# Performance work log

Measured on AMD Instinct MI355X. Metric: run time of the kernel, lower is better.

The kernel has to match this reference:

```python
import jax, jax.numpy as jnp
import numpy as np

N_EMBED = 1024
N_HEAD = 16
HEAD_DIM = N_EMBED // N_HEAD


def setup_inputs() -> dict:
    key = jax.random.key(0)
    ks = jax.random.split(key, 6)
    B, T, C = 4, 2048, N_EMBED
    scale = 1.0 / np.sqrt(C)
    x = jax.random.normal(ks[0], (B, T, C), dtype=jnp.float32)
    # torch nn.Linear weights are [out, in]; y = x @ W.T
    Wk = jax.random.normal(ks[1], (C, C), dtype=jnp.float32) * scale
    Wq = jax.random.normal(ks[2], (C, C), dtype=jnp.float32) * scale
    Wv = jax.random.normal(ks[3], (C, C), dtype=jnp.float32) * scale
    Wp = jax.random.normal(ks[4], (C, C), dtype=jnp.float32) * scale
    bp = jax.random.normal(ks[5], (C,), dtype=jnp.float32) * 0.01
    return {"x": x, "Wk": Wk, "Wq": Wq, "Wv": Wv, "Wp": Wp, "bp": bp}


def reference(x, Wk, Wq, Wv, Wp, bp):
    B, T, C = x.shape
    H, D = N_HEAD, HEAD_DIM
    # QKV projections (torch Linear: x @ W.T), split heads -> [B, H, T, D]
    k = (x @ Wk.T).reshape(B, T, H, D).transpose(0, 2, 1, 3)
    q = (x @ Wq.T).reshape(B, T, H, D).transpose(0, 2, 1, 3)
    v = (x @ Wv.T).reshape(B, T, H, D).transpose(0, 2, 1, 3)
    # scaled scores [B, H, T, T]
    att = jnp.einsum('bhtd,bhsd->bhts', q, k) * (1.0 / np.sqrt(D))
    causal = jnp.tril(jnp.ones((T, T), dtype=bool))
    att = jnp.where(causal[None, None, :, :], att, -jnp.inf)
    att = jax.nn.softmax(att, axis=-1)
    out = jnp.einsum('bhts,bhsd->bhtd', att, v)  # [B, H, T, D]
    out = out.transpose(0, 2, 1, 3).reshape(B, T, C)
    out = out @ Wp.T + bp
    return out
```

## Files before the change

### kernel.cpp

```cpp
#include <hip/hip_runtime.h>

typedef __bf16 bf16_t;
typedef bf16_t bf16x4 __attribute__((ext_vector_type(4)));
typedef bf16_t bf16x8 __attribute__((ext_vector_type(8)));
typedef float f32x4 __attribute__((ext_vector_type(4)));

#define B_ 4
#define T_ 2048
#define C_ 1024
#define H_ 16
#define D_ 64

#define GLDS(g, l)                                                          \
  __builtin_amdgcn_global_load_lds(                                         \
      (const __attribute__((address_space(1))) void*)(g),                   \
      (__attribute__((address_space(3))) void*)(l), 16, 0, 0)

static __device__ __forceinline__ f32x4 mfma16(bf16x8 a, bf16x8 b, f32x4 c) {
  return __builtin_amdgcn_mfma_f32_16x16x32_bf16(a, b, c, 0, 0, 0);
}

static __device__ __forceinline__ float exp2_hw(float x) {
  float r;
  asm("v_exp_f32 %0, %1" : "=v"(r) : "v"(x));
  return r;
}

__global__ void cvt_all(const float* __restrict__ x, const float* __restrict__ wq,
                        const float* __restrict__ wk, const float* __restrict__ wv,
                        const float* __restrict__ wp, bf16_t* __restrict__ xb,
                        bf16_t* __restrict__ wqb, bf16_t* __restrict__ wkb,
                        bf16_t* __restrict__ wvb, bf16_t* __restrict__ wpb) {
  int i = blockIdx.x * blockDim.x + threadIdx.x;
  const float* src;
  bf16_t* dst;
  int off;
  if (i < 2097152) {
    src = x; dst = xb; off = i;
  } else {
    int r = i - 2097152;
    int region = r >> 18;
    off = r & 262143;
    if (region == 0) { src = wq; dst = wqb; }
    else if (region == 1) { src = wk; dst = wkb; }
    else if (region == 2) { src = wv; dst = wvb; }
    else { src = wp; dst = wpb; }
  }
  float4 v = ((const float4*)src)[off];
  bf16x4 o = {(bf16_t)v.x, (bf16_t)v.y, (bf16_t)v.z, (bf16_t)v.w};
  ((bf16x4*)dst)[off] = o;
}

__global__ __launch_bounds__(512) void gemm_qkv(
    const bf16_t* __restrict__ xb, const bf16_t* __restrict__ wq,
    const bf16_t* __restrict__ wk, const bf16_t* __restrict__ wv,
    bf16_t* __restrict__ qo, bf16_t* __restrict__ ko, bf16_t* __restrict__ vt) {
  __shared__ bf16_t lA[2][128 * 64];
  __shared__ bf16_t lB[2][3][128 * 64];
  const int tid = threadIdx.x, wave = tid >> 6, lane = tid & 63;
  const int g = lane >> 4;
  const int bid = blockIdx.x;
  const int swz = ((bid & 7) << 6) | (bid >> 3);
  const int col0 = (swz & 7) * 128, row0 = (swz >> 3) * 128;
  const int wr = wave >> 2, wc = wave & 3;
  f32x4 acc[3][4][2] = {};

  const int soff[2] = {wave * 1024, (8 + wave) * 1024};
  size_t sgo[2];
#pragma unroll
  for (int i = 0; i < 2; ++i) {
    const int lin = soff[i] + lane * 16;
    const int r = lin >> 7;
    const int c = ((lin >> 4) & 7) ^ (r & 7);
    sgo[i] = (size_t)r * C_ + c * 8;
  }

#define QKV_STAGE(k0, b)                                                    \
  {                                                                         \
    _Pragma("unroll") for (int i = 0; i < 2; ++i) {                         \
      GLDS(xb + (size_t)row0 * C_ + (k0) + sgo[i], &lA[b][soff[i] >> 1]);   \
      GLDS(wq + (size_t)col0 * C_ + (k0) + sgo[i], &lB[b][0][soff[i] >> 1]);\
      GLDS(wk + (size_t)col0 * C_ + (k0) + sgo[i], &lB[b][1][soff[i] >> 1]);\
      GLDS(wv + (size_t)col0 * C_ + (k0) + sgo[i], &lB[b][2][soff[i] >> 1]);\
    }                                                                       \
  }

  QKV_STAGE(0, 0);
  int cur = 0;
  for (int k0 = 0; k0 < C_; k0 += 64) {
    __syncthreads();
    if (k0 + 64 < C_) QKV_STAGE(k0 + 64, cur ^ 1);
#pragma unroll
    for (int s = 0; s < 2; ++s) {
      const int c = s * 4 + g;
      bf16x8 af[4];
#pragma unroll
      for (int m = 0; m < 4; ++m) {
        const int r = wr * 64 + m * 16 + (lane & 15);
        af[m] = *(const bf16x8*)((const char*)lA[cur] + r * 128 +
                                 ((c ^ (r & 7)) << 4));
      }
#pragma unroll
      for (int z = 0; z < 3; ++z) {
        bf16x8 bfr[2];
#pragma unroll
        for (int n = 0; n < 2; ++n) {
          const int r = wc * 32 + n * 16 + (lane & 15);
          bfr[n] = *(const bf16x8*)((const char*)lB[cur][z] + r * 128 +
                                    ((c ^ (r & 7)) << 4));
        }
#pragma unroll
        for (int m = 0; m < 4; ++m)
#pragma unroll
          for (int n = 0; n < 2; ++n)
            acc[z][m][n] = mfma16(af[m], bfr[n], acc[z][m][n]);
      }
    }
    cur ^= 1;
  }
#pragma unroll
  for (int z = 0; z < 3; ++z) {
    bf16_t* outb = (z == 0) ? qo : ((z == 1) ? ko : vt);
    const float qs = (z == 0) ? 0.125f * 1.4426950408889634f : 1.0f;
#pragma unroll
    for (int m = 0; m < 4; ++m) {
#pragma unroll
      for (int n = 0; n < 2; ++n) {
        const int gr = row0 + wr * 64 + m * 16 + ((lane >> 4) << 2);
        const int gc = col0 + wc * 32 + n * 16 + (lane & 15);
        const int b = gr >> 11, t = gr & (T_ - 1);
        const int h = gc >> 6, d = gc & 63;
        if (z < 2) {
#pragma unroll
          for (int j = 0; j < 4; ++j)
            outb[(((size_t)(b * H_ + h)) * T_ + (t + j)) * D_ + d] =
                (bf16_t)(acc[z][m][n][j] * qs);
        } else {
          bf16x4 pk = {(bf16_t)acc[z][m][n][0], (bf16_t)acc[z][m][n][1],
                       (bf16_t)acc[z][m][n][2], (bf16_t)acc[z][m][n][3]};
          *(bf16x4*)(outb + (((size_t)(b * H_ + h)) * D_ + d) * T_ + t) = pk;
        }
      }
    }
  }
}

__global__ __launch_bounds__(256) void gemm_proj(const bf16_t* __restrict__ att,
                                                 const bf16_t* __restrict__ wp,
                                                 const float* __restrict__ bias,
                                                 float* __restrict__ out) {
  __shared__ bf16_t lA[2][128 * 64];
  __shared__ bf16_t lB[2][128 * 64];
  const int tid = threadIdx.x;
  const int wave = tid >> 6, lane = tid & 63;
  const int wr = wave >> 1, wc = wave & 1;
  const int row0 = blockIdx.y * 128, col0 = blockIdx.x * 128;
  f32x4 acc[4][4] = {};

  const int soff[4] = {wave * 1024, (4 + wave) * 1024, (8 + wave) * 1024,
                       (12 + wave) * 1024};
  size_t sgo[4];
#pragma unroll
  for (int i = 0; i < 4; ++i) {
    const int lin = soff[i] + lane * 16;
    const int r = lin >> 7;
    const int c = ((lin >> 4) & 7) ^ (r & 7);
    sgo[i] = (size_t)r * C_ + c * 8;
  }

#define PROJ_STAGE(k0, b)                                                   \
  {                                                                         \
    _Pragma("unroll") for (int i = 0; i < 4; ++i) {                         \
      GLDS(att + (size_t)row0 * C_ + (k0) + sgo[i], &lA[b][soff[i] >> 1]);  \
      GLDS(wp + (size_t)col0 * C_ + (k0) + sgo[i], &lB[b][soff[i] >> 1]);   \
    }                                                                       \
  }

  PROJ_STAGE(0, 0);
  int cur = 0;
  for (int k0 = 0; k0 < C_; k0 += 64) {
    __syncthreads();
    if (k0 + 64 < C_) PROJ_STAGE(k0 + 64, cur ^ 1);
#pragma unroll
    for (int s = 0; s < 2; ++s) {
      bf16x8 af[4], bfr[4];
#pragma unroll
      for (int m = 0; m < 4; ++m) {
        const int r = wr * 64 + m * 16 + (lane & 15);
        const int c = s * 4 + (lane >> 4);
        af[m] = *(const bf16x8*)((const char*)lA[cur] + r * 128 +
                                 ((c ^ (r & 7)) << 4));
      }
#pragma unroll
      for (int n = 0; n < 4; ++n) {
        const int r = wc * 64 + n * 16 + (lane & 15);
        const int c = s * 4 + (lane >> 4);
        bfr[n] = *(const bf16x8*)((const char*)lB[cur] + r * 128 +
                                  ((c ^ (r & 7)) << 4));
      }
#pragma unroll
      for (int m = 0; m < 4; ++m)
#pragma unroll
        for (int n = 0; n < 4; ++n) acc[m][n] = mfma16(af[m], bfr[n], acc[m][n]);
    }
    cur ^= 1;
  }
#pragma unroll
  for (int m = 0; m < 4; ++m) {
#pragma unroll
    for (int n = 0; n < 4; ++n) {
      const int gr = row0 + wr * 64 + m * 16 + ((lane >> 4) << 2);
      const int gc = col0 + wc * 64 + n * 16 + (lane & 15);
      const float bv = bias[gc];
#pragma unroll
      for (int j = 0; j < 4; ++j)
        out[(size_t)(gr + j) * C_ + gc] = acc[m][n][j] + bv;
    }
  }
}

__global__ __launch_bounds__(512, 4) void attn_fwd(
    const bf16_t* __restrict__ Q, const bf16_t* __restrict__ K,
    const bf16_t* __restrict__ V, bf16_t* __restrict__ AO) {
  __shared__ bf16_t lK[2][64 * 64];
  __shared__ bf16_t lV[2][64 * 64];
  __shared__ bf16_t lP[8][16 * 64];
  const int tid = threadIdx.x, wave = tid >> 6, lane = tid & 63;
  const int g = lane >> 4;
  const int bh = blockIdx.y;
  const size_t baseK = (size_t)bh * T_ * D_;
  const size_t baseV = (size_t)bh * D_ * T_;
  const int bb = bh >> 4, hh = bh & 15;

  int koff[2][4];
#pragma unroll
  for (int s = 0; s < 2; ++s)
#pragma unroll
    for (int nf = 0; nf < 4; ++nf) {
      const int r = nf * 16 + (lane & 15);
      const int c = s * 4 + g;
      koff[s][nf] = r * 128 + ((c ^ (r & 7)) << 4);
    }
  int pwoff[4];
  {
    const int r = lane & 15;
#pragma unroll
    for (int nf = 0; nf < 4; ++nf)
      pwoff[nf] = r * 128 + (((2 * nf + (g >> 1)) ^ (r & 7)) << 4) +
                  ((g & 1) << 3);
  }
  const int soff = wave * 1024;
  const int slin = soff + lane * 16;
  const int srow = slin >> 7;
  const int scol = ((slin >> 4) & 7) ^ (srow & 7);
  const size_t kgo = (size_t)srow * D_ + scol * 8;
  const size_t vgo = (size_t)srow * T_ + scol * 8;

  for (int half = 0; half < 2; ++half) {
    const int qt = half ? (15 - blockIdx.x) : blockIdx.x;
    const int twv = qt * 128 + wave * 16;
    const int ntiles = 2 * qt + 2;
    __syncthreads();
    GLDS(K + baseK + kgo, &lK[0][soff >> 1]);
    GLDS(V + baseV + vgo, &lV[0][soff >> 1]);
    bf16x8 qf[2];
#pragma unroll
    for (int s = 0; s < 2; ++s)
      qf[s] = *(const bf16x8*)(Q + baseK +
                               (size_t)(twv + (lane & 15)) * D_ + s * 32 +
                               (g << 3));
    float lrun = 0.f;
    f32x4 o[4] = {};
    int cur = 0;
    for (int it = 0; it < ntiles; ++it) {
      __syncthreads();
      if (it + 1 < ntiles) {
        const int nb = cur ^ 1;
        GLDS(K + baseK + (size_t)(it + 1) * 64 * D_ + kgo,
             &lK[nb][soff >> 1]);
        GLDS(V + baseV + (size_t)(it + 1) * 64 + vgo, &lV[nb][soff >> 1]);
      }
      const char* kb = (const char*)lK[cur];
      const char* vb = (const char*)lV[cur];
      const int s0 = it * 64;
      f32x4 sc[4];
#pragma unroll
      for (int nf = 0; nf < 4; ++nf) sc[nf] = (f32x4){};
      __builtin_amdgcn_s_setprio(1);
#pragma unroll
      for (int s = 0; s < 2; ++s)
#pragma unroll
        for (int nf = 0; nf < 4; ++nf)
          sc[nf] = mfma16(*(const bf16x8*)(kb + koff[s][nf]), qf[s], sc[nf]);
      __builtin_amdgcn_s_setprio(0);
      if (it >= 2 * qt) {
        const int t = twv + (lane & 15);
#pragma unroll
        for (int nf = 0; nf < 4; ++nf)
#pragma unroll
          for (int j = 0; j < 4; ++j) {
            const int s = s0 + nf * 16 + g * 4 + j;
            if (s > t) sc[nf][j] = -1e30f;
          }
      }
      bf16x4 pk[4];
      float psn[4];
#pragma unroll
      for (int nf = 0; nf < 4; ++nf) {
        float e0 = exp2_hw(sc[nf][0]);
        float e1 = exp2_hw(sc[nf][1]);
        float e2 = exp2_hw(sc[nf][2]);
        float e3 = exp2_hw(sc[nf][3]);
        pk[nf][0] = (bf16_t)e0;
        pk[nf][1] = (bf16_t)e1;
        pk[nf][2] = (bf16_t)e2;
        pk[nf][3] = (bf16_t)e3;
        psn[nf] = (e0 + e1) + (e2 + e3);
      }
      float ps = (psn[0] + psn[1]) + (psn[2] + psn[3]);
      ps += __shfl_xor(ps, 16);
      ps += __shfl_xor(ps, 32);
      lrun += ps;
      {
        char* pw = (char*)lP[wave];
#pragma unroll
        for (int nf = 0; nf < 4; ++nf) *(bf16x4*)(pw + pwoff[nf]) = pk[nf];
      }
      __builtin_amdgcn_s_setprio(1);
      const char* pb = (const char*)lP[wave];
#pragma unroll
      for (int s2 = 0; s2 < 2; ++s2) {
        bf16x8 pf = *(const bf16x8*)(pb + koff[s2][0]);
#pragma unroll
        for (int df = 0; df < 4; ++df)
          o[df] = mfma16(pf, *(const bf16x8*)(vb + koff[s2][df]), o[df]);
      }
      __builtin_amdgcn_s_setprio(0);
      cur ^= 1;
    }
    {
      const float inv = 1.0f / lrun;
      float ib[4];
#pragma unroll
      for (int j = 0; j < 4; ++j)
        ib[j] = __shfl(inv, (lane & 48) | ((g << 2) + j));
#pragma unroll
      for (int j = 0; j < 4; ++j) {
        const int t = twv + (g << 2) + j;
#pragma unroll
        for (int df = 0; df < 4; ++df) {
          const int cc = hh * 64 + df * 16 + (lane & 15);
          AO[((size_t)(bb * T_ + t)) * C_ + cc] = (bf16_t)(o[df][j] * ib[j]);
        }
      }
    }
  }
}

extern "C" void kernel_launch(void* const* d_in, const int* in_sizes, int n_in,
                              void* d_out, int out_size, void* d_ws,
                              size_t ws_size, hipStream_t stream) {
  const float* x = (const float*)d_in[0];
  const float* Wk = (const float*)d_in[1];
  const float* Wq = (const float*)d_in[2];
  const float* Wv = (const float*)d_in[3];
  const float* Wp = (const float*)d_in[4];
  const float* bp = (const float*)d_in[5];
  char* ws = (char*)d_ws;
  bf16_t* xb = (bf16_t*)ws;
  bf16_t* wqb = (bf16_t*)(ws + (16u << 20));
  bf16_t* wkb = (bf16_t*)(ws + (18u << 20));
  bf16_t* wvb = (bf16_t*)(ws + (20u << 20));
  bf16_t* wpb = (bf16_t*)(ws + (22u << 20));
  bf16_t* q = (bf16_t*)(ws + (24u << 20));
  bf16_t* k = (bf16_t*)(ws + (40u << 20));
  bf16_t* vt = (bf16_t*)(ws + (56u << 20));
  bf16_t* att = xb;

  cvt_all<<<12288, 256, 0, stream>>>(x, Wq, Wk, Wv, Wp, xb, wqb, wkb, wvb, wpb);
  gemm_qkv<<<512, 512, 0, stream>>>(xb, wqb, wkb, wvb, q, k, vt);
  attn_fwd<<<dim3(8, 64), 512, 0, stream>>>(q, k, vt, att);
  gemm_proj<<<dim3(8, 64), 256, 0, stream>>>(att, wpb, bp, (float*)d_out);
}
```

Before: 163.0 us.

## Halve QKV GEMM K-tile and use explicit vmcnt waits with two barriers

Shrinks the QKV projection GEMM's LDS tiles from K=64 to K=32, which halves shared memory per block, and adds a launch-bounds hint for 4 blocks per CU to raise occupancy. The LDS swizzle is recomputed for 64-byte rows and the per-fragment LDS offsets are hoisted out of the loop. The pipeline now issues the next stage's global-to-LDS loads, waits on vmcnt(4) so that only the current stage is guaranteed landed, and fences with raw s_barrier before and after compute instead of one __syncthreads. The trade is twice as many loop iterations and barriers per K sweep, plus a min-blocks hint that may cap registers for the 96-register accumulator.

```diff
diff --git a/kernel.cpp b/kernel.cpp
--- a/kernel.cpp
+++ b/kernel.cpp
@@ -51,12 +51,12 @@
   ((bf16x4*)dst)[off] = o;
 }
 
-__global__ __launch_bounds__(512) void gemm_qkv(
+__global__ __launch_bounds__(512, 4) void gemm_qkv(
     const bf16_t* __restrict__ xb, const bf16_t* __restrict__ wq,
     const bf16_t* __restrict__ wk, const bf16_t* __restrict__ wv,
     bf16_t* __restrict__ qo, bf16_t* __restrict__ ko, bf16_t* __restrict__ vt) {
-  __shared__ bf16_t lA[2][128 * 64];
-  __shared__ bf16_t lB[2][3][128 * 64];
+  __shared__ bf16_t lA[2][128 * 32];
+  __shared__ bf16_t lB[2][3][128 * 32];
   const int tid = threadIdx.x, wave = tid >> 6, lane = tid & 63;
   const int g = lane >> 4;
   const int bid = blockIdx.x;
@@ -65,50 +65,53 @@
   const int wr = wave >> 2, wc = wave & 3;
   f32x4 acc[3][4][2] = {};
 
-  const int soff[2] = {wave * 1024, (8 + wave) * 1024};
-  size_t sgo[2];
-#pragma unroll
-  for (int i = 0; i < 2; ++i) {
-    const int lin = soff[i] + lane * 16;
-    const int r = lin >> 7;
-    const int c = ((lin >> 4) & 7) ^ (r & 7);
-    sgo[i] = (size_t)r * C_ + c * 8;
+  const int soff = wave * 1024;
+  const int slin = soff + lane * 16;
+  const int srow = slin >> 6;
+  const int scol = ((slin >> 4) & 3) ^ ((srow >> 1) & 3);
+  const size_t sgo = (size_t)srow * C_ + scol * 8;
+
+  int aoff[4], boff[2];
+#pragma unroll
+  for (int m = 0; m < 4; ++m) {
+    const int r = wr * 64 + m * 16 + (lane & 15);
+    aoff[m] = r * 64 + ((g ^ ((r >> 1) & 3)) << 4);
+  }
+#pragma unroll
+  for (int n = 0; n < 2; ++n) {
+    const int r = wc * 32 + n * 16 + (lane & 15);
+    boff[n] = r * 64 + ((g ^ ((r >> 1) & 3)) << 4);
   }
 
 #define QKV_STAGE(k0, b)                                                    \
   {                                                                         \
-    _Pragma("unroll") for (int i = 0; i < 2; ++i) {                         \
-      GLDS(xb + (size_t)row0 * C_ + (k0) + sgo[i], &lA[b][soff[i] >> 1]);   \
-      GLDS(wq + (size_t)col0 * C_ + (k0) + sgo[i], &lB[b][0][soff[i] >> 1]);\
-      GLDS(wk + (size_t)col0 * C_ + (k0) + sgo[i], &lB[b][1][soff[i] >> 1]);\
-      GLDS(wv + (size_t)col0 * C_ + (k0) + sgo[i], &lB[b][2][soff[i] >> 1]);\
-    }                                                                       \
+    GLDS(xb + (size_t)row0 * C_ + (k0) + sgo, &lA[b][soff >> 1]);           \
+    GLDS(wq + (size_t)col0 * C_ + (k0) + sgo, &lB[b][0][soff >> 1]);        \
+    GLDS(wk + (size_t)col0 * C_ + (k0) + sgo, &lB[b][1][soff >> 1]);        \
+    GLDS(wv + (size_t)col0 * C_ + (k0) + sgo, &lB[b][2][soff >> 1]);        \
   }
 
   QKV_STAGE(0, 0);
   int cur = 0;
-  for (int k0 = 0; k0 < C_; k0 += 64) {
-    __syncthreads();
-    if (k0 + 64 < C_) QKV_STAGE(k0 + 64, cur ^ 1);
-#pragma unroll
-    for (int s = 0; s < 2; ++s) {
-      const int c = s * 4 + g;
+  for (int k0 = 32; k0 <= C_; k0 += 32) {
+    if (k0 < C_) {
+      QKV_STAGE(k0, cur ^ 1);
+      asm volatile("s_waitcnt vmcnt(4)" ::: "memory");
+    } else {
+      asm volatile("s_waitcnt vmcnt(0)" ::: "memory");
+    }
+    asm volatile("s_barrier" ::: "memory");
+    {
+      const char* ab = (const char*)lA[cur];
       bf16x8 af[4];
 #pragma unroll
-      for (int m = 0; m < 4; ++m) {
-        const int r = wr * 64 + m * 16 + (lane & 15);
-        af[m] = *(const bf16x8*)((const char*)lA[cur] + r * 128 +
-                                 ((c ^ (r & 7)) << 4));
-      }
+      for (int m = 0; m < 4; ++m) af[m] = *(const bf16x8*)(ab + aoff[m]);
 #pragma unroll
       for (int z = 0; z < 3; ++z) {
+        const char* bb = (const char*)lB[cur][z];
         bf16x8 bfr[2];
 #pragma unroll
-        for (int n = 0; n < 2; ++n) {
-          const int r = wc * 32 + n * 16 + (lane & 15);
-          bfr[n] = *(const bf16x8*)((const char*)lB[cur][z] + r * 128 +
-                                    ((c ^ (r & 7)) << 4));
-        }
+        for (int n = 0; n < 2; ++n) bfr[n] = *(const bf16x8*)(bb + boff[n]);
 #pragma unroll
         for (int m = 0; m < 4; ++m)
 #pragma unroll
@@ -116,6 +119,7 @@
             acc[z][m][n] = mfma16(af[m], bfr[n], acc[z][m][n]);
       }
     }
+    asm volatile("s_barrier" ::: "memory");
     cur ^= 1;
   }
 #pragma unroll
```

Measured after the change: 253.1 us. +55.2%, slower.

## Process 128-key tiles per iteration in attention, halving barrier and loop count

Applied to the files above, without the earlier changes.

Each attention loop iteration now loads and processes two 64-key K/V sub-tiles (128 keys) instead of one, so the causal loop runs qt+1 times instead of 2*qt+2. This halves the number of block-wide barriers and prefetch issue points per query tile, and gives more MFMA work between synchronisations. The cost is double-size K/V shared-memory buffers, which raises LDS per block and can lower the number of resident blocks per CU. It also raises register pressure because score fragments for both sub-tiles are live at once.

```diff
diff --git a/kernel.cpp b/kernel.cpp
--- a/kernel.cpp
+++ b/kernel.cpp
@@ -222,8 +222,8 @@
 __global__ __launch_bounds__(512, 4) void attn_fwd(
     const bf16_t* __restrict__ Q, const bf16_t* __restrict__ K,
     const bf16_t* __restrict__ V, bf16_t* __restrict__ AO) {
-  __shared__ bf16_t lK[2][64 * 64];
-  __shared__ bf16_t lV[2][64 * 64];
+  __shared__ bf16_t lK[2][2][64 * 64];
+  __shared__ bf16_t lV[2][2][64 * 64];
   __shared__ bf16_t lP[8][16 * 64];
   const int tid = threadIdx.x, wave = tid >> 6, lane = tid & 63;
   const int g = lane >> 4;
@@ -259,10 +259,13 @@
   for (int half = 0; half < 2; ++half) {
     const int qt = half ? (15 - blockIdx.x) : blockIdx.x;
     const int twv = qt * 128 + wave * 16;
-    const int ntiles = 2 * qt + 2;
+    const int ntiles = qt + 1;
     __syncthreads();
-    GLDS(K + baseK + kgo, &lK[0][soff >> 1]);
-    GLDS(V + baseV + vgo, &lV[0][soff >> 1]);
+#pragma unroll
+    for (int sub = 0; sub < 2; ++sub) {
+      GLDS(K + baseK + (size_t)sub * 64 * D_ + kgo, &lK[0][sub][soff >> 1]);
+      GLDS(V + baseV + (size_t)sub * 64 + vgo, &lV[0][sub][soff >> 1]);
+    }
     bf16x8 qf[2];
 #pragma unroll
     for (int s = 0; s < 2; ++s)
@@ -276,64 +279,81 @@
       __syncthreads();
       if (it + 1 < ntiles) {
         const int nb = cur ^ 1;
-        GLDS(K + baseK + (size_t)(it + 1) * 64 * D_ + kgo,
-             &lK[nb][soff >> 1]);
-        GLDS(V + baseV + (size_t)(it + 1) * 64 + vgo, &lV[nb][soff >> 1]);
-      }
-      const char* kb = (const char*)lK[cur];
-      const char* vb = (const char*)lV[cur];
-      const int s0 = it * 64;
-      f32x4 sc[4];
-#pragma unroll
-      for (int nf = 0; nf < 4; ++nf) sc[nf] = (f32x4){};
+        const size_t ks = (size_t)(it + 1) * 128;
+#pragma unroll
+        for (int sub = 0; sub < 2; ++sub) {
+          GLDS(K + baseK + (ks + sub * 64) * D_ + kgo,
+               &lK[nb][sub][soff >> 1]);
+          GLDS(V + baseV + ks + sub * 64 + vgo, &lV[nb][sub][soff >> 1]);
+        }
+      }
+      const int s0 = it * 128;
+      f32x4 sc[2][4];
+#pragma unroll
+      for (int sub = 0; sub < 2; ++sub)
+#pragma unroll
+        for (int nf = 0; nf < 4; ++nf) sc[sub][nf] = (f32x4){};
       __builtin_amdgcn_s_setprio(1);
 #pragma unroll
-      for (int s = 0; s < 2; ++s)
-#pragma unroll
-        for (int nf = 0; nf < 4; ++nf)
-          sc[nf] = mfma16(*(const bf16x8*)(kb + koff[s][nf]), qf[s], sc[nf]);
+      for (int sub = 0; sub < 2; ++sub) {
+        const char* kb = (const char*)lK[cur][sub];
+#pragma unroll
+        for (int s = 0; s < 2; ++s)
+#pragma unroll
+          for (int nf = 0; nf < 4; ++nf)
+            sc[sub][nf] =
+                mfma16(*(const bf16x8*)(kb + koff[s][nf]), qf[s], sc[sub][nf]);
+      }
       __builtin_amdgcn_s_setprio(0);
-      if (it >= 2 * qt) {
+      if (it == qt) {
         const int t = twv + (lane & 15);
 #pragma unroll
-        for (int nf = 0; nf < 4; ++nf)
-#pragma unroll
-          for (int j = 0; j < 4; ++j) {
-            const int s = s0 + nf * 16 + g * 4 + j;
-            if (s > t) sc[nf][j] = -1e30f;
-          }
-      }
-      bf16x4 pk[4];
-      float psn[4];
-#pragma unroll
-      for (int nf = 0; nf < 4; ++nf) {
-        float e0 = exp2_hw(sc[nf][0]);
-        float e1 = exp2_hw(sc[nf][1]);
-        float e2 = exp2_hw(sc[nf][2]);
-        float e3 = exp2_hw(sc[nf][3]);
-        pk[nf][0] = (bf16_t)e0;
-        pk[nf][1] = (bf16_t)e1;
-        pk[nf][2] = (bf16_t)e2;
-        pk[nf][3] = (bf16_t)e3;
-        psn[nf] = (e0 + e1) + (e2 + e3);
-      }
-      float ps = (psn[0] + psn[1]) + (psn[2] + psn[3]);
+        for (int sub = 0; sub < 2; ++sub)
+#pragma unroll
+          for (int nf = 0; nf < 4; ++nf)
+#pragma unroll
+            for (int j = 0; j < 4; ++j) {
+              const int s = s0 + sub * 64 + nf * 16 + g * 4 + j;
+              if (s > t) sc[sub][nf][j] = -1e30f;
+            }
+      }
+      float ps = 0.f;
+      bf16x4 pk[2][4];
+#pragma unroll
+      for (int sub = 0; sub < 2; ++sub) {
+        float psn[4];
+#pragma unroll
+        for (int nf = 0; nf < 4; ++nf) {
+          float e0 = exp2_hw(sc[sub][nf][0]);
+          float e1 = exp2_hw(sc[sub][nf][1]);
+          float e2 = exp2_hw(sc[sub][nf][2]);
+          float e3 = exp2_hw(sc[sub][nf][3]);
+          pk[sub][nf][0] = (bf16_t)e0;
+          pk[sub][nf][1] = (bf16_t)e1;
+          pk[sub][nf][2] = (bf16_t)e2;
+          pk[sub][nf][3] = (bf16_t)e3;
+          psn[nf] = (e0 + e1) + (e2 + e3);
+        }
+        ps += (psn[0] + psn[1]) + (psn[2] + psn[3]);
+      }
       ps += __shfl_xor(ps, 16);
       ps += __shfl_xor(ps, 32);
       lrun += ps;
-      {
+      __builtin_amdgcn_s_setprio(1);
+#pragma unroll
+      for (int sub = 0; sub < 2; ++sub) {
         char* pw = (char*)lP[wave];
 #pragma unroll
-        for (int nf = 0; nf < 4; ++nf) *(bf16x4*)(pw + pwoff[nf]) = pk[nf];
-      }
-      __builtin_amdgcn_s_setprio(1);
-      const char* pb = (const char*)lP[wave];
-#pragma unroll
-      for (int s2 = 0; s2 < 2; ++s2) {
-        bf16x8 pf = *(const bf16x8*)(pb + koff[s2][0]);
-#pragma unroll
-        for (int df = 0; df < 4; ++df)
-          o[df] = mfma16(pf, *(const bf16x8*)(vb + koff[s2][df]), o[df]);
+        for (int nf = 0; nf < 4; ++nf) *(bf16x4*)(pw + pwoff[nf]) = pk[sub][nf];
+        const char* pb = (const char*)lP[wave];
+        const char* vb = (const char*)lV[cur][sub];
+#pragma unroll
+        for (int s2 = 0; s2 < 2; ++s2) {
+          bf16x8 pf = *(const bf16x8*)(pb + koff[s2][0]);
+#pragma unroll
+          for (int df = 0; df < 4; ++df)
+            o[df] = mfma16(pf, *(const bf16x8*)(vb + koff[s2][df]), o[df]);
+        }
       }
       __builtin_amdgcn_s_setprio(0);
       cur ^= 1;
```

New measurement: 162.7 us. About the same (-0.2%).
